# Optimization experiments

Measured on AMD Instinct MI355X. Metric: run time of the kernel, lower is better.

The kernel has to match this reference:

```python
import jax, jax.numpy as jnp
import numpy as np

B, N, C, H = 1, 128, 128, 8
D = C // H
SCALE = D ** -0.5


def layer_norm(x, w, b, eps=1e-5):
    m = jnp.mean(x, axis=-1, keepdims=True)
    v = jnp.var(x, axis=-1, keepdims=True)
    return (x - m) * jax.lax.rsqrt(v + eps) * w + b


def setup_inputs() -> dict:
    key = jax.random.key(0)
    ks = jax.random.split(key, 8)
    s = 0.02
    return {
        "e": jax.random.normal(ks[0], (B, N, N, C), jnp.float32),
        "mask": jnp.zeros((B, N, N, 1), jnp.float32),
        "ln_w": jnp.ones((C,), jnp.float32),
        "ln_b": jnp.zeros((C,), jnp.float32),
        "w_qkv_in": jax.random.normal(ks[1], (C, 3 * C), jnp.float32) * s,
        "b_qkv_in": jnp.zeros((3 * C,), jnp.float32),
        "w_eg_in": jax.random.normal(ks[2], (C, 2 * H), jnp.float32) * s,
        "b_eg_in": jnp.zeros((2 * H,), jnp.float32),
        "w_qkv_out": jax.random.normal(ks[3], (C, 3 * C), jnp.float32) * s,
        "b_qkv_out": jnp.zeros((3 * C,), jnp.float32),
        "w_eg_out": jax.random.normal(ks[4], (C, 2 * H), jnp.float32) * s,
        "b_eg_out": jnp.zeros((2 * H,), jnp.float32),
        "w_o": jax.random.normal(ks[5], (2 * C, C), jnp.float32) * s,
        "b_o": jnp.zeros((C,), jnp.float32),
    }


def reference(e, mask, ln_w, ln_b, w_qkv_in, b_qkv_in, w_eg_in, b_eg_in,
              w_qkv_out, b_qkv_out, w_eg_out, b_eg_out, w_o, b_o):
    b, n = e.shape[0], e.shape[1]
    e_ln = layer_norm(e, ln_w, ln_b)

    # ---- incoming-edge stream ----
    qkv = e_ln @ w_qkv_in + b_qkv_in                      # [b,n,n,3C]
    Q, K, V = jnp.split(qkv, 3, axis=-1)
    Q = Q.reshape(b, n, n, D, H) * SCALE                  # bijdh
    K = K.reshape(b, n, n, D, H)
    V = V.reshape(b, n, n, D, H)
    eg = e_ln @ w_eg_in + b_eg_in                         # [b,n,n,2H]
    E_in = eg[..., :H][:, :, None, :, :]                  # [b,i,1,k,h]
    G_in = eg[..., H:][:, :, None, :, :]
    H_in = jnp.einsum('bijdh,bjkdh->bijkh', Q, K) + E_in
    mask_in = mask[:, :, None, :, :]                      # [b,i,1,k,1]
    gates_in = jax.nn.sigmoid(G_in + mask_in)
    A_in = jax.nn.softmax(H_in + mask_in, axis=3) * gates_in
    Va_in = jnp.einsum('bijkh,bjkdh->bijdh', A_in, V)

    # ---- outgoing-edge stream ----
    qkv = e_ln @ w_qkv_out + b_qkv_out
    Q, K, V = jnp.split(qkv, 3, axis=-1)
    Q = Q.reshape(b, n, n, D, H) * SCALE
    K = K.reshape(b, n, n, D, H)
    V = V.reshape(b, n, n, D, H)
    eg = e_ln @ w_eg_out + b_eg_out
    E_out = eg[..., :H][:, :, :, None, :]                 # [b,k,i,1,h]
    G_out = eg[..., H:][:, :, :, None, :]
    H_out = jnp.einsum('bijdh,bkjdh->bkijh', Q, K) + E_out
    mask_out = mask[:, :, :, None, :]                     # [b,k,i,1,1]
    gates_out = jax.nn.sigmoid(G_out + mask_out)
    A_out = jax.nn.softmax(H_out + mask_out, axis=1) * gates_out
    Va_out = jnp.einsum('bkijh,bkjdh->bijdh', A_out, V)

    Va = jnp.concatenate([Va_in, Va_out], axis=-1).reshape(b, n, n, 2 * C)
    return Va @ w_o + b_o
```

## Files before the change

### kernel.cpp

```cpp
#include <hip/hip_runtime.h>
#include <hip/hip_bf16.h>


#define NPOS 16384
#define CDIM 128

typedef __attribute__((ext_vector_type(8))) short bf16x8;
typedef __attribute__((ext_vector_type(8))) unsigned short u16x8;
typedef __attribute__((ext_vector_type(4))) float f32x4;

#define MFMA16(a, b, c) __builtin_amdgcn_mfma_f32_16x16x32_bf16((a), (b), (c), 0, 0, 0)

#define GLL16(gp, lp) __builtin_amdgcn_global_load_lds( \
    (const __attribute__((address_space(1))) void*)(gp), \
    (__attribute__((address_space(3))) void*)(lp), 16, 0, 0)

static __device__ __forceinline__ unsigned short f2bf(float x) {
    union { float f; unsigned int u; } v; v.f = x;
    unsigned int u = v.u;
    unsigned int r = u + 0x7FFFu + ((u >> 16) & 1u);
    return (unsigned short)(r >> 16);
}
static __device__ __forceinline__ float bf2f(unsigned short h) {
    union { float f; unsigned int u; } v; v.u = ((unsigned int)h) << 16; return v.f;
}

__global__ __launch_bounds__(256) void prep_kernel(
    const float* __restrict__ e, const float* __restrict__ lnw,
    const float* __restrict__ lnb, unsigned short* __restrict__ e_hl,
    const float* __restrict__ wq1, const float* __restrict__ we1,
    unsigned short* __restrict__ B1t,
    const float* __restrict__ wq2, const float* __restrict__ we2,
    unsigned short* __restrict__ B2t,
    const float* __restrict__ wo, unsigned short* __restrict__ B3t)
{
    const int t = threadIdx.x;
    const int bx = blockIdx.x;
    if (bx < 4096) {
        const int lane = t & 63;
        const int row = bx * 4 + (t >> 6);
        float2 x = *(const float2*)(e + (size_t)row * CDIM + lane * 2);
        float s = x.x + x.y, s2 = x.x * x.x + x.y * x.y;
        #pragma unroll
        for (int off = 1; off < 64; off <<= 1) {
            s  += __shfl_xor(s,  off, 64);
            s2 += __shfl_xor(s2, off, 64);
        }
        float m = s * (1.f / 128.f);
        float v = s2 * (1.f / 128.f) - m * m;
        float sc = rsqrtf(v + 1e-5f);
        float2 wv = *(const float2*)(lnw + lane * 2);
        float2 bv = *(const float2*)(lnb + lane * 2);
        float y0 = (x.x - m) * sc * wv.x + bv.x;
        float y1 = (x.y - m) * sc * wv.y + bv.y;
        unsigned short h0 = f2bf(y0), h1 = f2bf(y1);
        ushort2 hi = {h0, h1};
        ushort2 lo = {f2bf(y0 - bf2f(h0)), f2bf(y1 - bf2f(h1))};
        *(ushort2*)(e_hl + (size_t)row * 256 + lane * 2)       = hi;
        *(ushort2*)(e_hl + (size_t)row * 256 + 128 + lane * 2) = lo;
    } else if (bx < 4544) {
        int pb = bx - 4096;
        const float* wq; const float* we; unsigned short* Bt;
        if (pb < 224) { wq = wq1; we = we1; Bt = B1t; }
        else          { pb -= 224; wq = wq2; we = we2; Bt = B2t; }
        const int idx = pb * 256 + t;
        const int n = idx >> 7, k = idx & 127;
        float v = 0.f;
        if (n < 384) v = wq[(size_t)k * 384 + n];
        else if (n < 400) v = we[(size_t)k * 16 + (n - 384)];
        unsigned short hi = f2bf(v);
        Bt[idx] = hi;
        Bt[448 * 128 + idx] = f2bf(v - bf2f(hi));
    } else {
        const int idx = (bx - 4544) * 256 + t;
        const int n = idx >> 8, kp = idx & 255;
        const int d = kp & 15, pl = kp >> 4;
        const int k = d * 16 + pl;
        float v = wo[(size_t)k * 128 + n];
        unsigned short hi = f2bf(v);
        B3t[idx] = hi;
        B3t[128 * 256 + idx] = f2bf(v - bf2f(hi));
    }
}

__global__ __launch_bounds__(256) void gemm_qkv_kernel(
    const unsigned short* __restrict__ e_hl,
    const unsigned short* __restrict__ B1t, const unsigned short* __restrict__ B2t,
    const float* __restrict__ bq_i, const float* __restrict__ be_i,
    const float* __restrict__ bq_o, const float* __restrict__ be_o,
    const float* __restrict__ mask,
    unsigned short* __restrict__ QT, unsigned short* __restrict__ KT,
    unsigned short* __restrict__ VT,
    unsigned short* __restrict__ Etab, unsigned short* __restrict__ Gtab)
{
    __shared__ __align__(16) unsigned char smem[24576];
    unsigned short* Alds = (unsigned short*)smem;
    unsigned short* Blds = (unsigned short*)(smem + 16384);

    const int t = threadIdx.x;
    const int wave = t >> 6, lane = t & 63;
    const int m = lane & 15, q = lane >> 4;
    const int bx = blockIdx.x;
    const int W0blk = bx * 128;
    const int by = blockIdx.y;
    const int N0 = by * 64;
    const int br = blockIdx.z;
    const unsigned short* Bt = br ? B2t : B1t;
    const float* bias_qkv = br ? bq_o : bq_i;
    const float* bias_eg  = br ? be_o : be_i;

    f32x4 acc[2][4];
    #pragma unroll
    for (int a = 0; a < 2; ++a)
        #pragma unroll
        for (int c = 0; c < 4; ++c) acc[a][c] = (f32x4){0.f, 0.f, 0.f, 0.f};

    for (int kc = 0; kc < 4; ++kc) {
        #pragma unroll
        for (int ii = 0; ii < 6; ++ii) {
            const int id = wave + ii * 4;
            if (id < 16) {
                const int hl = id >> 3, s = id & 7;
                const int qq = s >> 1, rbase = (s & 1) * 64;
                const unsigned short* g = e_hl
                    + (size_t)(W0blk + rbase + lane) * 256 + hl * 128 + kc * 32 + qq * 8;
                unsigned short* l = Alds + hl * 4096 + qq * 1024 + rbase * 8;
                GLL16(g, l);
            } else {
                const int id2 = id - 16;
                const int hl = id2 >> 2, qq = id2 & 3;
                const unsigned short* g = Bt + (size_t)(N0 + lane) * 128
                    + hl * (448 * 128) + kc * 32 + qq * 8;
                unsigned short* l = Blds + hl * 2048 + qq * 512;
                GLL16(g, l);
            }
        }
        __syncthreads();

        bf16x8 aH[2], aL[2], bH[4], bL[4];
        #pragma unroll
        for (int ms = 0; ms < 2; ++ms) {
            const int row = wave * 32 + ms * 16 + m;
            aH[ms] = *(const bf16x8*)(Alds + 0    + q * 1024 + row * 8);
            aL[ms] = *(const bf16x8*)(Alds + 4096 + q * 1024 + row * 8);
        }
        #pragma unroll
        for (int ns = 0; ns < 4; ++ns) {
            bH[ns] = *(const bf16x8*)(Blds + 0    + q * 512 + (ns * 16 + m) * 8);
            bL[ns] = *(const bf16x8*)(Blds + 2048 + q * 512 + (ns * 16 + m) * 8);
        }
        #pragma unroll
        for (int ns = 0; ns < 4; ++ns) {
            acc[0][ns] = MFMA16(aH[0], bH[ns], acc[0][ns]);
            acc[1][ns] = MFMA16(aH[1], bH[ns], acc[1][ns]);
        }
        #pragma unroll
        for (int ns = 0; ns < 4; ++ns) {
            acc[0][ns] = MFMA16(aL[0], bH[ns], acc[0][ns]);
            acc[1][ns] = MFMA16(aL[1], bH[ns], acc[1][ns]);
        }
        #pragma unroll
        for (int ns = 0; ns < 4; ++ns) {
            acc[0][ns] = MFMA16(aH[0], bL[ns], acc[0][ns]);
            acc[1][ns] = MFMA16(aH[1], bL[ns], acc[1][ns]);
        }
        __syncthreads();
    }

    if (by < 6) {
        unsigned short (*Ts16)[66] = (unsigned short (*)[66])smem;
        #pragma unroll
        for (int ms = 0; ms < 2; ++ms)
            #pragma unroll
            for (int ns = 0; ns < 4; ++ns) {
                const int lc = ns * 16 + m;
                const int col = N0 + lc;
                const float bias = bias_qkv[col];
                const float scale = (col < 128) ? 0.25f : 1.f;
                #pragma unroll
                for (int r = 0; r < 4; ++r) {
                    const int lr = wave * 32 + ms * 16 + q * 4 + r;
                    Ts16[lr][lc] = f2bf((acc[ms][ns][r] + bias) * scale);
                }
            }
        __syncthreads();
        const int qsel = by >> 1, dhalf = by & 1;
        unsigned short* dstH = (qsel == 0) ? QT : (qsel == 1 ? KT : VT);
        #pragma unroll
        for (int it = 0; it < 4; ++it) {
            int item = it * 256 + t;
            int hh = item >> 7, lr = item & 127;
            u16x8 hi;
            #pragma unroll
            for (int dd = 0; dd < 8; ++dd)
                hi[dd] = Ts16[lr][dd * 8 + hh];
            size_t addr = (((size_t)(br * 8 + hh) * 2 + dhalf) * NPOS
                           + (size_t)bx * 128 + lr) * 8;
            *(u16x8*)(dstH + addr) = hi;
        }
    } else {
        float* Tf = (float*)smem;
        #pragma unroll
        for (int ms = 0; ms < 2; ++ms) {
            const float bias = bias_eg[m];
            #pragma unroll
            for (int r = 0; r < 4; ++r) {
                const int lr = wave * 32 + ms * 16 + q * 4 + r;
                Tf[lr * 33 + m] = acc[ms][0][r] + bias;
            }
        }
        __syncthreads();
        const int r128 = t & 127, grp = t >> 7;
        const float mk = mask[bx * 128 + r128];
        const int dst = br ? (r128 * 128 + bx) : (bx * 128 + r128);
        if (grp == 0) {
            #pragma unroll
            for (int h = 0; h < 8; ++h)
                Etab[(size_t)(br * 8 + h) * NPOS + dst] =
                    f2bf(Tf[r128 * 33 + h] + mk);
        } else {
            #pragma unroll
            for (int h = 0; h < 8; ++h) {
                const float g = Tf[r128 * 33 + 8 + h] + mk;
                Gtab[(size_t)(br * 8 + h) * NPOS + dst] =
                    f2bf(1.f / (1.f + __expf(-g)));
            }
        }
    }
}

__global__ __launch_bounds__(256) void transpose_kernel(
    unsigned short* __restrict__ QT, unsigned short* __restrict__ KT,
    unsigned short* __restrict__ VT)
{
    const int s = blockIdx.y;
    unsigned short* base;
    int sub;
    if (s < 32)       { base = QT; sub = s; }
    else if (s < 48)  { base = KT; sub = 16 + (s - 32); }
    else              { base = VT; sub = 16 + (s - 48); }
    unsigned short* P = base + (size_t)sub * NPOS * 8;

    int x = blockIdx.x, a = 0;
    while (x >= 8 - a) { x -= 8 - a; ++a; }
    const int b = a + x;

    __shared__ unsigned short T1[16][136];
    __shared__ unsigned short T2[16][136];

    const int t = threadIdx.x;
    const int r = t >> 4, c = t & 15;

    u16x8 v1 = *(const u16x8*)(P + ((size_t)(a * 16 + r) * 128 + b * 16 + c) * 8);
    *(u16x8*)&T1[r][c * 8] = v1;
    if (a != b) {
        u16x8 v2 = *(const u16x8*)(P + ((size_t)(b * 16 + r) * 128 + a * 16 + c) * 8);
        *(u16x8*)&T2[r][c * 8] = v2;
    }
    __syncthreads();

    u16x8 w1 = *(const u16x8*)&T1[c][r * 8];
    *(u16x8*)(P + ((size_t)(b * 16 + r) * 128 + a * 16 + c) * 8) = w1;
    if (a != b) {
        u16x8 w2 = *(const u16x8*)&T2[c][r * 8];
        *(u16x8*)(P + ((size_t)(a * 16 + r) * 128 + b * 16 + c) * 8) = w2;
    }
}

__global__ __launch_bounds__(256) void gemm_out_kernel(
    const float* __restrict__ va,
    const unsigned short* __restrict__ B3t,
    const float* __restrict__ bias,
    float* __restrict__ out)
{
    const int t = threadIdx.x;
    const int wave = t >> 6, lane = t & 63;
    const int m = lane & 15, q = lane >> 4;
    const int W0 = blockIdx.x * 64 + wave * 16;
    const int N0 = blockIdx.y * 64;

    f32x4 acc[4];
    #pragma unroll
    for (int c = 0; c < 4; ++c) acc[c] = (f32x4){0.f, 0.f, 0.f, 0.f};

    const float* arow = va + (size_t)(W0 + m) * 256;
    const unsigned short* bcol[4];
    #pragma unroll
    for (int ns = 0; ns < 4; ++ns)
        bcol[ns] = B3t + (size_t)(N0 + ns * 16 + m) * 256;

    #pragma unroll 2
    for (int kc = 0; kc < 8; ++kc) {
        const int ko = kc * 32 + q * 8;
        const float4* ap = (const float4*)(arow + ko);
        float4 f0 = ap[0], f1 = ap[1];
        float xs[8] = {f0.x, f0.y, f0.z, f0.w, f1.x, f1.y, f1.z, f1.w};
        bf16x8 ah, al;
        #pragma unroll
        for (int jj = 0; jj < 8; ++jj) {
            unsigned short h = f2bf(xs[jj]);
            ah[jj] = (short)h;
            al[jj] = (short)f2bf(xs[jj] - bf2f(h));
        }
        bf16x8 bh[4], bl[4];
        #pragma unroll
        for (int ns = 0; ns < 4; ++ns) {
            bh[ns] = *(const bf16x8*)(bcol[ns] + ko);
            bl[ns] = *(const bf16x8*)(bcol[ns] + 128 * 256 + ko);
        }
        #pragma unroll
        for (int ns = 0; ns < 4; ++ns) acc[ns] = MFMA16(ah, bh[ns], acc[ns]);
        #pragma unroll
        for (int ns = 0; ns < 4; ++ns) acc[ns] = MFMA16(al, bh[ns], acc[ns]);
        #pragma unroll
        for (int ns = 0; ns < 4; ++ns) acc[ns] = MFMA16(ah, bl[ns], acc[ns]);
    }

    #pragma unroll
    for (int ns = 0; ns < 4; ++ns) {
        const int col = N0 + ns * 16 + m;
        #pragma unroll
        for (int r = 0; r < 4; ++r) {
            const int prow = W0 + q * 4 + r;
            const int orow = ((prow & 127) << 7) | (prow >> 7);
            out[(size_t)orow * 128 + col] = acc[ns][r] + bias[col];
        }
    }
}

__global__ __launch_bounds__(256) void attn_kernel(
    const unsigned short* __restrict__ QT, const unsigned short* __restrict__ KT,
    const unsigned short* __restrict__ VT,
    const unsigned short* __restrict__ Etab, const unsigned short* __restrict__ Gtab,
    float* __restrict__ va)
{
    const int j = blockIdx.x, h = blockIdx.y, br = blockIdx.z;
    const int t = threadIdx.x;
    const int wave = t >> 6, lane = t & 63;
    const int m = lane & 15, q = lane >> 4;
    const int plane = br * 8 + h;
    const size_t SP = (size_t)NPOS * 8;
    const size_t jb = (size_t)j * 128 * 8;
    const unsigned short* __restrict__ Eb = Etab + (size_t)plane * NPOS;
    const unsigned short* __restrict__ Gb = Gtab + (size_t)plane * NPOS;

    __shared__ unsigned short Vth[16 * 136];
    __shared__ unsigned short Pl[128 * 136];

    const int strip = wave * 32;

    f32x4 S[2][8];
    #pragma unroll
    for (int mt = 0; mt < 2; ++mt)
        #pragma unroll
        for (int r = 0; r < 4; ++r) {
            const int i = strip + mt * 16 + q * 4 + r;
            u16x8 ev = *(const u16x8*)(Eb + (size_t)i * 128 + m * 8);
            #pragma unroll
            for (int nt = 0; nt < 8; ++nt) S[mt][nt][r] = bf2f(ev[nt]);
        }

    {
        int c = t >> 1, ch = t & 1;
        int krow = (c & 15) * 8 + (c >> 4);
        const unsigned short* src = VT + (size_t)(plane * 2 + ch) * SP + jb
                                  + (size_t)krow * 8;
        u16x8 v = *(const u16x8*)src;
        #pragma unroll
        for (int dd = 0; dd < 8; ++dd)
            Vth[(ch * 8 + dd) * 136 + c] = v[dd];
    }

    const bf16x8 zero8 = {};
    const int hf = q & 1;
    const size_t qko = (size_t)(plane * 2 + hf) * SP + jb;

    bf16x8 aQ[2];
    #pragma unroll
    for (int mt = 0; mt < 2; ++mt) {
        const size_t off = qko + (size_t)(strip + mt * 16 + m) * 8;
        aQ[mt] = (q < 2) ? *(const bf16x8*)(QT + off) : zero8;
    }

    #pragma unroll
    for (int nt = 0; nt < 8; ++nt) {
        const size_t koff = qko + (size_t)(m * 8 + nt) * 8;
        bf16x8 bK = (q < 2) ? *(const bf16x8*)(KT + koff) : zero8;
        #pragma unroll
        for (int mt = 0; mt < 2; ++mt)
            S[mt][nt] = MFMA16(aQ[mt], bK, S[mt][nt]);
    }

    #pragma unroll
    for (int mt = 0; mt < 2; ++mt)
        #pragma unroll
        for (int r = 0; r < 4; ++r) {
            float v = -1e30f;
            #pragma unroll
            for (int nt = 0; nt < 8; ++nt) v = fmaxf(v, S[mt][nt][r]);
            v = fmaxf(v, __shfl_xor(v, 1)); v = fmaxf(v, __shfl_xor(v, 2));
            v = fmaxf(v, __shfl_xor(v, 4)); v = fmaxf(v, __shfl_xor(v, 8));
            float s = 0.f;
            #pragma unroll
            for (int nt = 0; nt < 8; ++nt) {
                float p = __expf(S[mt][nt][r] - v);
                S[mt][nt][r] = p;
                s += p;
            }
            s += __shfl_xor(s, 1); s += __shfl_xor(s, 2);
            s += __shfl_xor(s, 4); s += __shfl_xor(s, 8);
            const float inv = 1.f / s;
            const int i = strip + mt * 16 + q * 4 + r;
            u16x8 gv = *(const u16x8*)(Gb + (size_t)i * 128 + m * 8);
            #pragma unroll
            for (int nt = 0; nt < 4; ++nt) {
                Pl[i * 136 + nt * 16 + m] =
                    f2bf(S[mt][nt][r] * inv * bf2f(gv[nt]));
                Pl[i * 136 + (nt + 4) * 16 + m] =
                    f2bf(S[mt][nt + 4][r] * inv * bf2f(gv[nt + 4]));
            }
        }

    __syncthreads();

    f32x4 av[2] = {(f32x4){0.f, 0.f, 0.f, 0.f}, (f32x4){0.f, 0.f, 0.f, 0.f}};
    #pragma unroll
    for (int kc = 0; kc < 4; ++kc) {
        const int off = kc * 32 + q * 8;
        bf16x8 bV = *(const bf16x8*)&Vth[m * 136 + off];
        #pragma unroll
        for (int mt = 0; mt < 2; ++mt) {
            bf16x8 aP = *(const bf16x8*)&Pl[(strip + mt * 16 + m) * 136 + off];
            av[mt] = MFMA16(aP, bV, av[mt]);
        }
    }

    #pragma unroll
    for (int mt = 0; mt < 2; ++mt)
        #pragma unroll
        for (int r = 0; r < 4; ++r) {
            const int i = strip + mt * 16 + q * 4 + r;
            va[((size_t)(j * 128 + i)) * 256 + plane * 16 + m] = av[mt][r];
        }
}

extern "C" void kernel_launch(void* const* d_in, const int* in_sizes, int n_in,
                              void* d_out, int out_size, void* d_ws, size_t ws_size,
                              hipStream_t stream) {
    const float* e        = (const float*)d_in[0];
    const float* mask     = (const float*)d_in[1];
    const float* ln_w     = (const float*)d_in[2];
    const float* ln_b     = (const float*)d_in[3];
    const float* w_qkv_in = (const float*)d_in[4];
    const float* b_qkv_in = (const float*)d_in[5];
    const float* w_eg_in  = (const float*)d_in[6];
    const float* b_eg_in  = (const float*)d_in[7];
    const float* w_qkv_o  = (const float*)d_in[8];
    const float* b_qkv_o  = (const float*)d_in[9];
    const float* w_eg_o   = (const float*)d_in[10];
    const float* b_eg_o   = (const float*)d_in[11];
    const float* w_o      = (const float*)d_in[12];
    const float* b_o      = (const float*)d_in[13];
    float* out = (float*)d_out;

    char* base = (char*)d_ws;
    const size_t PLANE = (size_t)16 * NPOS * 16;
    unsigned short* e_hl = (unsigned short*)base;
    unsigned short* QT = (unsigned short*)(base + (size_t)NPOS * 256 * 2);
    unsigned short* KT = QT + PLANE;
    unsigned short* VT = KT + PLANE;
    float* va = (float*)(VT + PLANE);
    unsigned short* Etab = (unsigned short*)(va + (size_t)NPOS * 256);
    unsigned short* Gtab = Etab + (size_t)16 * NPOS;
    unsigned short* B3t  = Gtab + (size_t)16 * NPOS;

    unsigned short* B1t = (unsigned short*)va;
    unsigned short* B2t = B1t + (size_t)2 * 448 * 128;

    prep_kernel<<<4672, 256, 0, stream>>>(
        e, ln_w, ln_b, e_hl,
        w_qkv_in, w_eg_in, B1t, w_qkv_o, w_eg_o, B2t, w_o, B3t);

    gemm_qkv_kernel<<<dim3(128, 7, 2), 256, 0, stream>>>(
        e_hl, B1t, B2t, b_qkv_in, b_eg_in, b_qkv_o, b_eg_o, mask,
        QT, KT, VT, Etab, Gtab);

    transpose_kernel<<<dim3(36, 64), 256, 0, stream>>>(QT, KT, VT);

    attn_kernel<<<dim3(128, 8, 2), 256, 0, stream>>>(
        QT, KT, VT, Etab, Gtab, va);

    gemm_out_kernel<<<dim3(256, 2), 256, 0, stream>>>(va, B3t, b_o, out);
}
```

Measured before the change: 172.6 us.

## Fuse transpose into QKV GEMM epilogue and widen output GEMM tile

Drops the separate in-place transpose kernel. The QKV GEMM epilogue now writes the transposed position layout directly for Q and for the outgoing-branch K/V, which saves a full read-modify-write pass over those tensors and one launch. Block x indices are swizzled so neighbouring blocks write scattered, transposed rows, which trades write coalescing for this saving. The output GEMM now computes all 128 columns per block (8 accumulator tiles), halving the grid and reusing each A-row conversion, at the cost of more registers.

Result: faster. 167.7 us (-2.8%).

```diff
diff --git a/kernel.cpp b/kernel.cpp
--- a/kernel.cpp
+++ b/kernel.cpp
@@ -100,7 +100,8 @@
     const int t = threadIdx.x;
     const int wave = t >> 6, lane = t & 63;
     const int m = lane & 15, q = lane >> 4;
-    const int bx = blockIdx.x;
+    const int c = blockIdx.x;
+    const int bx = ((c & 31) << 2) | (c >> 5);
     const int W0blk = bx * 128;
     const int by = blockIdx.y;
     const int N0 = by * 64;
@@ -113,7 +114,7 @@
     #pragma unroll
     for (int a = 0; a < 2; ++a)
         #pragma unroll
-        for (int c = 0; c < 4; ++c) acc[a][c] = (f32x4){0.f, 0.f, 0.f, 0.f};
+        for (int cc = 0; cc < 4; ++cc) acc[a][cc] = (f32x4){0.f, 0.f, 0.f, 0.f};
 
     for (int kc = 0; kc < 4; ++kc) {
         #pragma unroll
@@ -186,6 +187,7 @@
         __syncthreads();
         const int qsel = by >> 1, dhalf = by & 1;
         unsigned short* dstH = (qsel == 0) ? QT : (qsel == 1 ? KT : VT);
+        const bool tr = (qsel == 0) || (br == 1);
         #pragma unroll
         for (int it = 0; it < 4; ++it) {
             int item = it * 256 + t;
@@ -194,9 +196,10 @@
             #pragma unroll
             for (int dd = 0; dd < 8; ++dd)
                 hi[dd] = Ts16[lr][dd * 8 + hh];
-            size_t addr = (((size_t)(br * 8 + hh) * 2 + dhalf) * NPOS
-                           + (size_t)bx * 128 + lr) * 8;
-            *(u16x8*)(dstH + addr) = hi;
+            const size_t sub = ((size_t)(br * 8 + hh) * 2 + dhalf) * NPOS;
+            const size_t p16 = tr ? ((size_t)lr * 128 + bx)
+                                  : ((size_t)bx * 128 + lr);
+            *(u16x8*)(dstH + (sub + p16) * 8) = hi;
         }
     } else {
         float* Tf = (float*)smem;
@@ -226,44 +229,6 @@
                     f2bf(1.f / (1.f + __expf(-g)));
             }
         }
-    }
-}
-
-__global__ __launch_bounds__(256) void transpose_kernel(
-    unsigned short* __restrict__ QT, unsigned short* __restrict__ KT,
-    unsigned short* __restrict__ VT)
-{
-    const int s = blockIdx.y;
-    unsigned short* base;
-    int sub;
-    if (s < 32)       { base = QT; sub = s; }
-    else if (s < 48)  { base = KT; sub = 16 + (s - 32); }
-    else              { base = VT; sub = 16 + (s - 48); }
-    unsigned short* P = base + (size_t)sub * NPOS * 8;
-
-    int x = blockIdx.x, a = 0;
-    while (x >= 8 - a) { x -= 8 - a; ++a; }
-    const int b = a + x;
-
-    __shared__ unsigned short T1[16][136];
-    __shared__ unsigned short T2[16][136];
-
-    const int t = threadIdx.x;
-    const int r = t >> 4, c = t & 15;
-
-    u16x8 v1 = *(const u16x8*)(P + ((size_t)(a * 16 + r) * 128 + b * 16 + c) * 8);
-    *(u16x8*)&T1[r][c * 8] = v1;
-    if (a != b) {
-        u16x8 v2 = *(const u16x8*)(P + ((size_t)(b * 16 + r) * 128 + a * 16 + c) * 8);
-        *(u16x8*)&T2[r][c * 8] = v2;
-    }
-    __syncthreads();
-
-    u16x8 w1 = *(const u16x8*)&T1[c][r * 8];
-    *(u16x8*)(P + ((size_t)(b * 16 + r) * 128 + a * 16 + c) * 8) = w1;
-    if (a != b) {
-        u16x8 w2 = *(const u16x8*)&T2[c][r * 8];
-        *(u16x8*)(P + ((size_t)(a * 16 + r) * 128 + b * 16 + c) * 8) = w2;
     }
 }
 
@@ -277,17 +242,13 @@
     const int wave = t >> 6, lane = t & 63;
     const int m = lane & 15, q = lane >> 4;
     const int W0 = blockIdx.x * 64 + wave * 16;
-    const int N0 = blockIdx.y * 64;
-
-    f32x4 acc[4];
-    #pragma unroll
-    for (int c = 0; c < 4; ++c) acc[c] = (f32x4){0.f, 0.f, 0.f, 0.f};
+
+    f32x4 acc[8];
+    #pragma unroll
+    for (int cc = 0; cc < 8; ++cc) acc[cc] = (f32x4){0.f, 0.f, 0.f, 0.f};
 
     const float* arow = va + (size_t)(W0 + m) * 256;
-    const unsigned short* bcol[4];
-    #pragma unroll
-    for (int ns = 0; ns < 4; ++ns)
-        bcol[ns] = B3t + (size_t)(N0 + ns * 16 + m) * 256;
+    const unsigned short* brow = B3t + (size_t)m * 256;
 
     #pragma unroll 2
     for (int kc = 0; kc < 8; ++kc) {
@@ -302,23 +263,24 @@
             ah[jj] = (short)h;
             al[jj] = (short)f2bf(xs[jj] - bf2f(h));
         }
-        bf16x8 bh[4], bl[4];
-        #pragma unroll
-        for (int ns = 0; ns < 4; ++ns) {
-            bh[ns] = *(const bf16x8*)(bcol[ns] + ko);
-            bl[ns] = *(const bf16x8*)(bcol[ns] + 128 * 256 + ko);
-        }
-        #pragma unroll
-        for (int ns = 0; ns < 4; ++ns) acc[ns] = MFMA16(ah, bh[ns], acc[ns]);
-        #pragma unroll
-        for (int ns = 0; ns < 4; ++ns) acc[ns] = MFMA16(al, bh[ns], acc[ns]);
-        #pragma unroll
-        for (int ns = 0; ns < 4; ++ns) acc[ns] = MFMA16(ah, bl[ns], acc[ns]);
-    }
-
-    #pragma unroll
-    for (int ns = 0; ns < 4; ++ns) {
-        const int col = N0 + ns * 16 + m;
+        bf16x8 bh[8], bl[8];
+        #pragma unroll
+        for (int ns = 0; ns < 8; ++ns) {
+            const unsigned short* bp = brow + (size_t)ns * (16 * 256) + ko;
+            bh[ns] = *(const bf16x8*)bp;
+            bl[ns] = *(const bf16x8*)(bp + 128 * 256);
+        }
+        #pragma unroll
+        for (int ns = 0; ns < 8; ++ns) acc[ns] = MFMA16(ah, bh[ns], acc[ns]);
+        #pragma unroll
+        for (int ns = 0; ns < 8; ++ns) acc[ns] = MFMA16(al, bh[ns], acc[ns]);
+        #pragma unroll
+        for (int ns = 0; ns < 8; ++ns) acc[ns] = MFMA16(ah, bl[ns], acc[ns]);
+    }
+
+    #pragma unroll
+    for (int ns = 0; ns < 8; ++ns) {
+        const int col = ns * 16 + m;
         #pragma unroll
         for (int r = 0; r < 4; ++r) {
             const int prow = W0 + q * 4 + r;
@@ -485,10 +447,8 @@
         e_hl, B1t, B2t, b_qkv_in, b_eg_in, b_qkv_o, b_eg_o, mask,
         QT, KT, VT, Etab, Gtab);
 
-    transpose_kernel<<<dim3(36, 64), 256, 0, stream>>>(QT, KT, VT);
-
     attn_kernel<<<dim3(128, 8, 2), 256, 0, stream>>>(
         QT, KT, VT, Etab, Gtab, va);
 
-    gemm_out_kernel<<<dim3(256, 2), 256, 0, stream>>>(va, B3t, b_o, out);
-}
+    gemm_out_kernel<<<256, 256, 0, stream>>>(va, B3t, b_o, out);
+}
```
